# Performance work log

Measured on AMD Instinct MI355X. Metric: run time of the kernel, lower is better.

## Reference

```python
import jax, jax.numpy as jnp
import numpy as np

D_MODEL = 1024
N_HEADS = 16
HEAD_DIM = D_MODEL // N_HEADS  # 64
SCALE = HEAD_DIM ** -0.5       # nn.Parameter, frozen since lsa=False


def setup_inputs() -> dict:
    key = jax.random.key(0)
    kq, kk, kv = jax.random.split(key, 3)
    bs, h, s, d = 4, N_HEADS, 2048, HEAD_DIM
    q = jax.random.normal(kq, (bs, h, s, d), dtype=jnp.float32)
    k = jax.random.normal(kk, (bs, h, d, s), dtype=jnp.float32)  # pre-transposed like torch input
    v = jax.random.normal(kv, (bs, h, s, d), dtype=jnp.float32)
    return {"q": q, "k": k, "v": v}


def reference(q, k, v):
    # attn_scores: [bs, n_heads, q_len, seq_len]
    scale = jnp.asarray(SCALE, dtype=q.dtype)
    attn_scores = jnp.einsum('bhqd,bhds->bhqs', q, k) * scale
    # prev=None, attn_mask=None, key_padding_mask=None; dropout p=0.0 -> identity
    attn_weights = jax.nn.softmax(attn_scores, axis=-1)
    output = jnp.einsum('bhqs,bhsd->bhqd', attn_weights, v)
    return output, attn_weights
```

## Files before the change

### kernel.cpp

```cpp
#include <hip/hip_runtime.h>


#define S_LEN 2048
#define DH 64
#define NHEADS 64

typedef short short8 __attribute__((ext_vector_type(8)));
typedef float f32x4 __attribute__((ext_vector_type(4)));
typedef float f32x16 __attribute__((ext_vector_type(16)));
typedef unsigned short u16;

__device__ __forceinline__ u16 f2bf(float f) {
  union { float f; unsigned u; } x;
  x.f = f;
  unsigned r = x.u + 0x7fffu + ((x.u >> 16) & 1u);
  return (u16)(r >> 16);
}

__device__ __forceinline__ unsigned pkbf(float a, float b) {
  return (unsigned)f2bf(a) | ((unsigned)f2bf(b) << 16);
}

__device__ __forceinline__ void plswap(unsigned& a, unsigned& b) {
  asm("v_permlane32_swap_b32 %0, %1" : "+v"(a), "+v"(b));
}

__global__ __launch_bounds__(256) void cvt_scale_k(const float* __restrict__ in,
                                                   u16* __restrict__ out,
                                                   float scale, int n4) {
  int i = blockIdx.x * 256 + threadIdx.x;
  if (i >= n4) return;
  float4 v = ((const float4*)in)[i];
  union { u16 s[4]; unsigned long long ll; } o;
  o.s[0] = f2bf(v.x * scale); o.s[1] = f2bf(v.y * scale);
  o.s[2] = f2bf(v.z * scale); o.s[3] = f2bf(v.w * scale);
  ((unsigned long long*)out)[i] = o.ll;
}

__global__ __launch_bounds__(256) void transpose_cvt_k(const float* __restrict__ in,
                                                       u16* __restrict__ out,
                                                       int R, int C) {
  __shared__ float tile[64][65];
  const int tilesC = C >> 6;
  const int tilesPerHead = (R >> 6) * tilesC;
  int hb = blockIdx.x;
  int head = hb / tilesPerHead;
  int t = hb - head * tilesPerHead;
  int tr = t / tilesC, tc = t - tr * tilesC;
  const float* ip = in + (size_t)head * R * C + (size_t)tr * 64 * C + (size_t)tc * 64;
  u16* op = out + (size_t)head * R * C + (size_t)tc * 64 * R + (size_t)tr * 64;
  int c = threadIdx.x & 63, r0 = threadIdx.x >> 6;
#pragma unroll
  for (int k = 0; k < 16; ++k) {
    int r = (k << 2) + r0;
    tile[r][c] = ip[(size_t)r * C + c];
  }
  __syncthreads();
#pragma unroll
  for (int k = 0; k < 16; ++k) {
    int orow = (k << 2) + r0;
    op[(size_t)orow * R + c] = f2bf(tile[c][orow]);
  }
}

__global__ __launch_bounds__(256, 4) void attn_k(const u16* __restrict__ Qb,
                                                 const u16* __restrict__ Kn,
                                                 const u16* __restrict__ Vt,
                                                 float* __restrict__ Og,
                                                 float* __restrict__ Pg) {
  __shared__ float tile[4][32 * 32];
  int bid = blockIdx.x;
  int work = ((bid & 7) << 7) | (bid >> 3);
  int head = work >> 4;
  int rblk = work & 15;
  int lane = threadIdx.x & 63;
  int wv = threadIdx.x >> 6;
  int q = lane & 31;
  int hi = lane >> 5;
  int q0 = (rblk << 7) + (wv << 5);
  float* tw = tile[wv];
  int rq = lane >> 3;
  int rc = lane & 7;

  const u16* qp = Qb + (size_t)(head * S_LEN + q0 + q) * DH + hi * 8;
  short8 qf0 = *(const short8*)(qp);
  short8 qf1 = *(const short8*)(qp + 16);
  short8 qf2 = *(const short8*)(qp + 32);
  short8 qf3 = *(const short8*)(qp + 48);

  const u16* kp = Kn + (size_t)head * S_LEN * DH + (size_t)q * DH + hi * 8;
  const u16* vp = Vt + (size_t)head * DH * S_LEN + (size_t)q * S_LEN + hi * 8;

  float ls0 = 0.f, ls1 = 0.f, ls2 = 0.f, ls3 = 0.f;
  for (int j0 = 0; j0 < S_LEN; j0 += 32) {
    const u16* kb = kp + (size_t)j0 * DH;
    short8 k0 = *(const short8*)(kb);
    short8 k1 = *(const short8*)(kb + 16);
    short8 k2 = *(const short8*)(kb + 32);
    short8 k3 = *(const short8*)(kb + 48);
    f32x16 s = {};
    s = __builtin_amdgcn_mfma_f32_32x32x16_bf16(k0, qf0, s, 0, 0, 0);
    s = __builtin_amdgcn_mfma_f32_32x32x16_bf16(k1, qf1, s, 0, 0, 0);
    s = __builtin_amdgcn_mfma_f32_32x32x16_bf16(k2, qf2, s, 0, 0, 0);
    s = __builtin_amdgcn_mfma_f32_32x32x16_bf16(k3, qf3, s, 0, 0, 0);
#pragma unroll
    for (int r = 0; r < 16; r += 4) {
      ls0 += __expf(s[r]);
      ls1 += __expf(s[r + 1]);
      ls2 += __expf(s[r + 2]);
      ls3 += __expf(s[r + 3]);
    }
  }
  float ls = (ls0 + ls1) + (ls2 + ls3);
  ls += __shfl_xor(ls, 32);
  float rl = 1.f / ls;

  f32x16 oa = {}, ob = {};
  float* pbW = Pg + (size_t)(head * S_LEN + q0) * S_LEN;

  for (int j0 = 0; j0 < S_LEN; j0 += 32) {
    const u16* kb = kp + (size_t)j0 * DH;
    short8 k0 = *(const short8*)(kb);
    short8 k1 = *(const short8*)(kb + 16);
    short8 k2 = *(const short8*)(kb + 32);
    short8 k3 = *(const short8*)(kb + 48);
    const u16* vj = vp + j0;
    short8 v0 = *(const short8*)(vj);
    short8 v1 = *(const short8*)(vj + 16);
    short8 v2 = *(const short8*)(vj + 32 * S_LEN);
    short8 v3 = *(const short8*)(vj + 32 * S_LEN + 16);

    f32x16 s = {};
    s = __builtin_amdgcn_mfma_f32_32x32x16_bf16(k0, qf0, s, 0, 0, 0);
    s = __builtin_amdgcn_mfma_f32_32x32x16_bf16(k1, qf1, s, 0, 0, 0);
    s = __builtin_amdgcn_mfma_f32_32x32x16_bf16(k2, qf2, s, 0, 0, 0);
    s = __builtin_amdgcn_mfma_f32_32x32x16_bf16(k3, qf3, s, 0, 0, 0);

    float p[16];
#pragma unroll
    for (int r = 0; r < 16; ++r) p[r] = __expf(s[r]) * rl;

#pragma unroll
    for (int g = 0; g < 4; ++g) {
      int phys = (2 * g + hi) ^ (q & 7);
      f32x4 w = {p[4 * g], p[4 * g + 1], p[4 * g + 2], p[4 * g + 3]};
      *(f32x4*)&tw[q * 32 + phys * 4] = w;
    }

    unsigned A0 = pkbf(p[0], p[1]),   A1 = pkbf(p[2], p[3]);
    unsigned B0 = pkbf(p[4], p[5]),   B1 = pkbf(p[6], p[7]);
    plswap(A0, B0);
    plswap(A1, B1);
    unsigned C0 = pkbf(p[8], p[9]),   C1 = pkbf(p[10], p[11]);
    unsigned D0 = pkbf(p[12], p[13]), D1 = pkbf(p[14], p[15]);
    plswap(C0, D0);
    plswap(C1, D1);
    union { unsigned w[4]; short8 v; } pa0u = {{A0, A1, B0, B1}};
    union { unsigned w[4]; short8 v; } pa1u = {{C0, C1, D0, D1}};

    oa = __builtin_amdgcn_mfma_f32_32x32x16_bf16(pa0u.v, v0, oa, 0, 0, 0);
    oa = __builtin_amdgcn_mfma_f32_32x32x16_bf16(pa1u.v, v1, oa, 0, 0, 0);
    ob = __builtin_amdgcn_mfma_f32_32x32x16_bf16(pa0u.v, v2, ob, 0, 0, 0);
    ob = __builtin_amdgcn_mfma_f32_32x32x16_bf16(pa1u.v, v3, ob, 0, 0, 0);

    float* ps = pbW + j0;
#pragma unroll
    for (int g = 0; g < 4; ++g) {
      int qi = 8 * g + rq;
      int phys = rc ^ (qi & 7);
      f32x4 v = *(const f32x4*)&tw[qi * 32 + phys * 4];
      __builtin_nontemporal_store(v, (f32x4*)(ps + (size_t)qi * S_LEN + rc * 4));
    }
  }

  float* ogb = Og + (size_t)(head * S_LEN + q0) * DH;
#pragma unroll
  for (int r = 0; r < 16; ++r) {
    int qi = (r & 3) + 8 * (r >> 2) + 4 * hi;
    tw[qi * 32 + q] = oa[r];
  }
#pragma unroll
  for (int g = 0; g < 4; ++g) {
    int qi = 8 * g + rq;
    f32x4 v = *(const f32x4*)&tw[qi * 32 + rc * 4];
    __builtin_nontemporal_store(v, (f32x4*)(ogb + (size_t)qi * DH + rc * 4));
  }
#pragma unroll
  for (int r = 0; r < 16; ++r) {
    int qi = (r & 3) + 8 * (r >> 2) + 4 * hi;
    tw[qi * 32 + q] = ob[r];
  }
#pragma unroll
  for (int g = 0; g < 4; ++g) {
    int qi = 8 * g + rq;
    f32x4 v = *(const f32x4*)&tw[qi * 32 + rc * 4];
    __builtin_nontemporal_store(v, (f32x4*)(ogb + (size_t)qi * DH + 32 + rc * 4));
  }
}

extern "C" void kernel_launch(void* const* d_in, const int* in_sizes, int n_in,
                              void* d_out, int out_size, void* d_ws, size_t ws_size,
                              hipStream_t stream) {
  const float* q = (const float*)d_in[0];
  const float* k = (const float*)d_in[1];
  const float* v = (const float*)d_in[2];
  float* Og = (float*)d_out;
  float* Pg = Og + (size_t)NHEADS * S_LEN * DH;

  const size_t elems = (size_t)NHEADS * S_LEN * DH;
  u16* Qb = (u16*)d_ws;
  u16* Kn = Qb + elems;
  u16* Vt = Kn + elems;

  int n4 = (int)(elems / 4);
  cvt_scale_k<<<n4 / 256, 256, 0, stream>>>(q, Qb, 0.125f, n4);
  transpose_cvt_k<<<NHEADS * (S_LEN / 64), 256, 0, stream>>>(k, Kn, DH, S_LEN);
  transpose_cvt_k<<<NHEADS * (S_LEN / 64), 256, 0, stream>>>(v, Vt, S_LEN, DH);
  attn_k<<<NHEADS * (S_LEN / 128), 256, 0, stream>>>(Qb, Kn, Vt, Og, Pg);
}
```

Before: 406.5 us.

## Add dedicated store wavefront streaming attention probabilities from double-buffered LDS

Adds a fifth wavefront per block that only copies the softmax probability tiles from shared memory to global memory. The four compute wavefronts write their tiles into a double-buffered LDS area between two block barriers per iteration. The goal is to take the large global probability writes off the compute wavefronts' instruction stream so they overlap with the MFMA work. In exchange, it adds two block-wide barriers per key tile, doubles LDS use and concentrates all store issue in a single wavefront, which can become the limiter.

```diff
diff --git a/kernel.cpp b/kernel.cpp
--- a/kernel.cpp
+++ b/kernel.cpp
@@ -63,24 +63,46 @@
   }
 }
 
-__global__ __launch_bounds__(256, 4) void attn_k(const u16* __restrict__ Qb,
+__global__ __launch_bounds__(320, 5) void attn_k(const u16* __restrict__ Qb,
                                                  const u16* __restrict__ Kn,
                                                  const u16* __restrict__ Vt,
                                                  float* __restrict__ Og,
                                                  float* __restrict__ Pg) {
-  __shared__ float tile[4][32 * 32];
+  __shared__ float buf[2][4][32 * 32];
   int bid = blockIdx.x;
   int work = ((bid & 7) << 7) | (bid >> 3);
   int head = work >> 4;
   int rblk = work & 15;
   int lane = threadIdx.x & 63;
   int wv = threadIdx.x >> 6;
+  int rq = lane >> 3;
+  int rc = lane & 7;
+
+  if (wv == 4) {
+    float* pgb = Pg + ((size_t)head * S_LEN + (size_t)rblk * 128) * S_LEN;
+    for (int t = 0; t < 64; ++t) {
+      __syncthreads();
+      __syncthreads();
+      int j0 = t << 5;
+      const float* tb = &buf[t & 1][0][0];
+#pragma unroll
+      for (int w = 0; w < 4; ++w) {
+#pragma unroll
+        for (int g = 0; g < 4; ++g) {
+          int qi = 8 * g + rq;
+          int phys = rc ^ (qi & 7);
+          f32x4 v = *(const f32x4*)&tb[(w * 1024) + qi * 32 + phys * 4];
+          __builtin_nontemporal_store(
+              v, (f32x4*)(pgb + (size_t)(w * 32 + qi) * S_LEN + j0 + rc * 4));
+        }
+      }
+    }
+    return;
+  }
+
   int q = lane & 31;
   int hi = lane >> 5;
   int q0 = (rblk << 7) + (wv << 5);
-  float* tw = tile[wv];
-  int rq = lane >> 3;
-  int rc = lane & 7;
 
   const u16* qp = Qb + (size_t)(head * S_LEN + q0 + q) * DH + hi * 8;
   short8 qf0 = *(const short8*)(qp);
@@ -116,9 +138,9 @@
   float rl = 1.f / ls;
 
   f32x16 oa = {}, ob = {};
-  float* pbW = Pg + (size_t)(head * S_LEN + q0) * S_LEN;
-
-  for (int j0 = 0; j0 < S_LEN; j0 += 32) {
+
+  for (int t = 0; t < 64; ++t) {
+    int j0 = t << 5;
     const u16* kb = kp + (size_t)j0 * DH;
     short8 k0 = *(const short8*)(kb);
     short8 k1 = *(const short8*)(kb + 16);
@@ -140,12 +162,17 @@
 #pragma unroll
     for (int r = 0; r < 16; ++r) p[r] = __expf(s[r]) * rl;
 
+    __syncthreads();
+
+    float* tw = &buf[t & 1][wv][0];
 #pragma unroll
     for (int g = 0; g < 4; ++g) {
       int phys = (2 * g + hi) ^ (q & 7);
       f32x4 w = {p[4 * g], p[4 * g + 1], p[4 * g + 2], p[4 * g + 3]};
       *(f32x4*)&tw[q * 32 + phys * 4] = w;
     }
+
+    __syncthreads();
 
     unsigned A0 = pkbf(p[0], p[1]),   A1 = pkbf(p[2], p[3]);
     unsigned B0 = pkbf(p[4], p[5]),   B1 = pkbf(p[6], p[7]);
@@ -162,38 +189,30 @@
     oa = __builtin_amdgcn_mfma_f32_32x32x16_bf16(pa1u.v, v1, oa, 0, 0, 0);
     ob = __builtin_amdgcn_mfma_f32_32x32x16_bf16(pa0u.v, v2, ob, 0, 0, 0);
     ob = __builtin_amdgcn_mfma_f32_32x32x16_bf16(pa1u.v, v3, ob, 0, 0, 0);
-
-    float* ps = pbW + j0;
-#pragma unroll
-    for (int g = 0; g < 4; ++g) {
-      int qi = 8 * g + rq;
-      int phys = rc ^ (qi & 7);
-      f32x4 v = *(const f32x4*)&tw[qi * 32 + phys * 4];
-      __builtin_nontemporal_store(v, (f32x4*)(ps + (size_t)qi * S_LEN + rc * 4));
-    }
-  }
-
+  }
+
+  float* te = &buf[0][wv][0];
   float* ogb = Og + (size_t)(head * S_LEN + q0) * DH;
 #pragma unroll
   for (int r = 0; r < 16; ++r) {
     int qi = (r & 3) + 8 * (r >> 2) + 4 * hi;
-    tw[qi * 32 + q] = oa[r];
+    te[qi * 32 + q] = oa[r];
   }
 #pragma unroll
   for (int g = 0; g < 4; ++g) {
     int qi = 8 * g + rq;
-    f32x4 v = *(const f32x4*)&tw[qi * 32 + rc * 4];
+    f32x4 v = *(const f32x4*)&te[qi * 32 + rc * 4];
     __builtin_nontemporal_store(v, (f32x4*)(ogb + (size_t)qi * DH + rc * 4));
   }
 #pragma unroll
   for (int r = 0; r < 16; ++r) {
     int qi = (r & 3) + 8 * (r >> 2) + 4 * hi;
-    tw[qi * 32 + q] = ob[r];
+    te[qi * 32 + q] = ob[r];
   }
 #pragma unroll
   for (int g = 0; g < 4; ++g) {
     int qi = 8 * g + rq;
-    f32x4 v = *(const f32x4*)&tw[qi * 32 + rc * 4];
+    f32x4 v = *(const f32x4*)&te[qi * 32 + rc * 4];
     __builtin_nontemporal_store(v, (f32x4*)(ogb + (size_t)qi * DH + 32 + rc * 4));
   }
 }
@@ -216,5 +235,5 @@
   cvt_scale_k<<<n4 / 256, 256, 0, stream>>>(q, Qb, 0.125f, n4);
   transpose_cvt_k<<<NHEADS * (S_LEN / 64), 256, 0, stream>>>(k, Kn, DH, S_LEN);
   transpose_cvt_k<<<NHEADS * (S_LEN / 64), 256, 0, stream>>>(v, Vt, S_LEN, DH);
-  attn_k<<<NHEADS * (S_LEN / 128), 256, 0, stream>>>(Qb, Kn, Vt, Og, Pg);
-}
+  attn_k<<<NHEADS * (S_LEN / 128), 320, 0, stream>>>(Qb, Kn, Vt, Og, Pg);
+}
```

After: 466.8 us. +14.8%, slower.

## Process two query tiles per block, fusing second tile's row-sum pass into first's

Applied to the files above, without the earlier changes.

Each block now handles two 128-row query groups. The softmax-denominator pass for the second group is computed inside the first group's output loop, reusing the same K fragments, and the second group then runs its own output pass. This removes one separate QK^T sweep per pair of tiles and halves the grid, at the cost of higher register pressure (launch bounds lowered to 2 blocks) and fewer blocks for latency hiding.

```diff
diff --git a/kernel.cpp b/kernel.cpp
--- a/kernel.cpp
+++ b/kernel.cpp
@@ -63,35 +63,41 @@
   }
 }
 
-__global__ __launch_bounds__(256, 4) void attn_k(const u16* __restrict__ Qb,
+__global__ __launch_bounds__(256, 2) void attn_k(const u16* __restrict__ Qb,
                                                  const u16* __restrict__ Kn,
                                                  const u16* __restrict__ Vt,
                                                  float* __restrict__ Og,
                                                  float* __restrict__ Pg) {
   __shared__ float tile[4][32 * 32];
   int bid = blockIdx.x;
-  int work = ((bid & 7) << 7) | (bid >> 3);
-  int head = work >> 4;
-  int rblk = work & 15;
+  int work = ((bid & 7) << 6) | (bid >> 3);
+  int head = work >> 3;
+  int rblk = work & 7;
   int lane = threadIdx.x & 63;
   int wv = threadIdx.x >> 6;
   int q = lane & 31;
   int hi = lane >> 5;
-  int q0 = (rblk << 7) + (wv << 5);
+  int q0A = (rblk << 8) + (wv << 5);
+  int q0B = q0A + 128;
   float* tw = tile[wv];
   int rq = lane >> 3;
   int rc = lane & 7;
 
-  const u16* qp = Qb + (size_t)(head * S_LEN + q0 + q) * DH + hi * 8;
-  short8 qf0 = *(const short8*)(qp);
-  short8 qf1 = *(const short8*)(qp + 16);
-  short8 qf2 = *(const short8*)(qp + 32);
-  short8 qf3 = *(const short8*)(qp + 48);
+  const u16* qpA = Qb + (size_t)(head * S_LEN + q0A + q) * DH + hi * 8;
+  short8 qa0 = *(const short8*)(qpA);
+  short8 qa1 = *(const short8*)(qpA + 16);
+  short8 qa2 = *(const short8*)(qpA + 32);
+  short8 qa3 = *(const short8*)(qpA + 48);
+  const u16* qpB = Qb + (size_t)(head * S_LEN + q0B + q) * DH + hi * 8;
+  short8 qb0 = *(const short8*)(qpB);
+  short8 qb1 = *(const short8*)(qpB + 16);
+  short8 qb2 = *(const short8*)(qpB + 32);
+  short8 qb3 = *(const short8*)(qpB + 48);
 
   const u16* kp = Kn + (size_t)head * S_LEN * DH + (size_t)q * DH + hi * 8;
   const u16* vp = Vt + (size_t)head * DH * S_LEN + (size_t)q * S_LEN + hi * 8;
 
-  float ls0 = 0.f, ls1 = 0.f, ls2 = 0.f, ls3 = 0.f;
+  float la0 = 0.f, la1 = 0.f, la2 = 0.f, la3 = 0.f;
   for (int j0 = 0; j0 < S_LEN; j0 += 32) {
     const u16* kb = kp + (size_t)j0 * DH;
     short8 k0 = *(const short8*)(kb);
@@ -99,24 +105,25 @@
     short8 k2 = *(const short8*)(kb + 32);
     short8 k3 = *(const short8*)(kb + 48);
     f32x16 s = {};
-    s = __builtin_amdgcn_mfma_f32_32x32x16_bf16(k0, qf0, s, 0, 0, 0);
-    s = __builtin_amdgcn_mfma_f32_32x32x16_bf16(k1, qf1, s, 0, 0, 0);
-    s = __builtin_amdgcn_mfma_f32_32x32x16_bf16(k2, qf2, s, 0, 0, 0);
-    s = __builtin_amdgcn_mfma_f32_32x32x16_bf16(k3, qf3, s, 0, 0, 0);
+    s = __builtin_amdgcn_mfma_f32_32x32x16_bf16(k0, qa0, s, 0, 0, 0);
+    s = __builtin_amdgcn_mfma_f32_32x32x16_bf16(k1, qa1, s, 0, 0, 0);
+    s = __builtin_amdgcn_mfma_f32_32x32x16_bf16(k2, qa2, s, 0, 0, 0);
+    s = __builtin_amdgcn_mfma_f32_32x32x16_bf16(k3, qa3, s, 0, 0, 0);
 #pragma unroll
     for (int r = 0; r < 16; r += 4) {
-      ls0 += __expf(s[r]);
-      ls1 += __expf(s[r + 1]);
-      ls2 += __expf(s[r + 2]);
-      ls3 += __expf(s[r + 3]);
-    }
-  }
-  float ls = (ls0 + ls1) + (ls2 + ls3);
-  ls += __shfl_xor(ls, 32);
-  float rl = 1.f / ls;
+      la0 += __expf(s[r]);
+      la1 += __expf(s[r + 1]);
+      la2 += __expf(s[r + 2]);
+      la3 += __expf(s[r + 3]);
+    }
+  }
+  float lsA = (la0 + la1) + (la2 + la3);
+  lsA += __shfl_xor(lsA, 32);
+  float rlA = 1.f / lsA;
 
   f32x16 oa = {}, ob = {};
-  float* pbW = Pg + (size_t)(head * S_LEN + q0) * S_LEN;
+  float lb0 = 0.f, lb1 = 0.f, lb2 = 0.f, lb3 = 0.f;
+  float* pbA = Pg + (size_t)(head * S_LEN + q0A) * S_LEN;
 
   for (int j0 = 0; j0 < S_LEN; j0 += 32) {
     const u16* kb = kp + (size_t)j0 * DH;
@@ -131,14 +138,14 @@
     short8 v3 = *(const short8*)(vj + 32 * S_LEN + 16);
 
     f32x16 s = {};
-    s = __builtin_amdgcn_mfma_f32_32x32x16_bf16(k0, qf0, s, 0, 0, 0);
-    s = __builtin_amdgcn_mfma_f32_32x32x16_bf16(k1, qf1, s, 0, 0, 0);
-    s = __builtin_amdgcn_mfma_f32_32x32x16_bf16(k2, qf2, s, 0, 0, 0);
-    s = __builtin_amdgcn_mfma_f32_32x32x16_bf16(k3, qf3, s, 0, 0, 0);
+    s = __builtin_amdgcn_mfma_f32_32x32x16_bf16(k0, qa0, s, 0, 0, 0);
+    s = __builtin_amdgcn_mfma_f32_32x32x16_bf16(k1, qa1, s, 0, 0, 0);
+    s = __builtin_amdgcn_mfma_f32_32x32x16_bf16(k2, qa2, s, 0, 0, 0);
+    s = __builtin_amdgcn_mfma_f32_32x32x16_bf16(k3, qa3, s, 0, 0, 0);
 
     float p[16];
 #pragma unroll
-    for (int r = 0; r < 16; ++r) p[r] = __expf(s[r]) * rl;
+    for (int r = 0; r < 16; ++r) p[r] = __expf(s[r]) * rlA;
 
 #pragma unroll
     for (int g = 0; g < 4; ++g) {
@@ -163,7 +170,7 @@
     ob = __builtin_amdgcn_mfma_f32_32x32x16_bf16(pa0u.v, v2, ob, 0, 0, 0);
     ob = __builtin_amdgcn_mfma_f32_32x32x16_bf16(pa1u.v, v3, ob, 0, 0, 0);
 
-    float* ps = pbW + j0;
+    float* ps = pbA + j0;
 #pragma unroll
     for (int g = 0; g < 4; ++g) {
       int qi = 8 * g + rq;
@@ -171,9 +178,22 @@
       f32x4 v = *(const f32x4*)&tw[qi * 32 + phys * 4];
       __builtin_nontemporal_store(v, (f32x4*)(ps + (size_t)qi * S_LEN + rc * 4));
     }
-  }
-
-  float* ogb = Og + (size_t)(head * S_LEN + q0) * DH;
+
+    f32x16 sb = {};
+    sb = __builtin_amdgcn_mfma_f32_32x32x16_bf16(k0, qb0, sb, 0, 0, 0);
+    sb = __builtin_amdgcn_mfma_f32_32x32x16_bf16(k1, qb1, sb, 0, 0, 0);
+    sb = __builtin_amdgcn_mfma_f32_32x32x16_bf16(k2, qb2, sb, 0, 0, 0);
+    sb = __builtin_amdgcn_mfma_f32_32x32x16_bf16(k3, qb3, sb, 0, 0, 0);
+#pragma unroll
+    for (int r = 0; r < 16; r += 4) {
+      lb0 += __expf(sb[r]);
+      lb1 += __expf(sb[r + 1]);
+      lb2 += __expf(sb[r + 2]);
+      lb3 += __expf(sb[r + 3]);
+    }
+  }
+
+  float* ogA = Og + (size_t)(head * S_LEN + q0A) * DH;
 #pragma unroll
   for (int r = 0; r < 16; ++r) {
     int qi = (r & 3) + 8 * (r >> 2) + 4 * hi;
@@ -183,7 +203,7 @@
   for (int g = 0; g < 4; ++g) {
     int qi = 8 * g + rq;
     f32x4 v = *(const f32x4*)&tw[qi * 32 + rc * 4];
-    __builtin_nontemporal_store(v, (f32x4*)(ogb + (size_t)qi * DH + rc * 4));
+    __builtin_nontemporal_store(v, (f32x4*)(ogA + (size_t)qi * DH + rc * 4));
   }
 #pragma unroll
   for (int r = 0; r < 16; ++r) {
@@ -194,7 +214,94 @@
   for (int g = 0; g < 4; ++g) {
     int qi = 8 * g + rq;
     f32x4 v = *(const f32x4*)&tw[qi * 32 + rc * 4];
-    __builtin_nontemporal_store(v, (f32x4*)(ogb + (size_t)qi * DH + 32 + rc * 4));
+    __builtin_nontemporal_store(v, (f32x4*)(ogA + (size_t)qi * DH + 32 + rc * 4));
+  }
+
+  float lsB = (lb0 + lb1) + (lb2 + lb3);
+  lsB += __shfl_xor(lsB, 32);
+  float rlB = 1.f / lsB;
+
+  oa = (f32x16){};
+  ob = (f32x16){};
+  float* pbB = Pg + (size_t)(head * S_LEN + q0B) * S_LEN;
+
+  for (int j0 = 0; j0 < S_LEN; j0 += 32) {
+    const u16* kb = kp + (size_t)j0 * DH;
+    short8 k0 = *(const short8*)(kb);
+    short8 k1 = *(const short8*)(kb + 16);
+    short8 k2 = *(const short8*)(kb + 32);
+    short8 k3 = *(const short8*)(kb + 48);
+    const u16* vj = vp + j0;
+    short8 v0 = *(const short8*)(vj);
+    short8 v1 = *(const short8*)(vj + 16);
+    short8 v2 = *(const short8*)(vj + 32 * S_LEN);
+    short8 v3 = *(const short8*)(vj + 32 * S_LEN + 16);
+
+    f32x16 s = {};
+    s = __builtin_amdgcn_mfma_f32_32x32x16_bf16(k0, qb0, s, 0, 0, 0);
+    s = __builtin_amdgcn_mfma_f32_32x32x16_bf16(k1, qb1, s, 0, 0, 0);
+    s = __builtin_amdgcn_mfma_f32_32x32x16_bf16(k2, qb2, s, 0, 0, 0);
+    s = __builtin_amdgcn_mfma_f32_32x32x16_bf16(k3, qb3, s, 0, 0, 0);
+
+    float p[16];
+#pragma unroll
+    for (int r = 0; r < 16; ++r) p[r] = __expf(s[r]) * rlB;
+
+#pragma unroll
+    for (int g = 0; g < 4; ++g) {
+      int phys = (2 * g + hi) ^ (q & 7);
+      f32x4 w = {p[4 * g], p[4 * g + 1], p[4 * g + 2], p[4 * g + 3]};
+      *(f32x4*)&tw[q * 32 + phys * 4] = w;
+    }
+
+    unsigned A0 = pkbf(p[0], p[1]),   A1 = pkbf(p[2], p[3]);
+    unsigned B0 = pkbf(p[4], p[5]),   B1 = pkbf(p[6], p[7]);
+    plswap(A0, B0);
+    plswap(A1, B1);
+    unsigned C0 = pkbf(p[8], p[9]),   C1 = pkbf(p[10], p[11]);
+    unsigned D0 = pkbf(p[12], p[13]), D1 = pkbf(p[14], p[15]);
+    plswap(C0, D0);
+    plswap(C1, D1);
+    union { unsigned w[4]; short8 v; } pa0u = {{A0, A1, B0, B1}};
+    union { unsigned w[4]; short8 v; } pa1u = {{C0, C1, D0, D1}};
+
+    oa = __builtin_amdgcn_mfma_f32_32x32x16_bf16(pa0u.v, v0, oa, 0, 0, 0);
+    oa = __builtin_amdgcn_mfma_f32_32x32x16_bf16(pa1u.v, v1, oa, 0, 0, 0);
+    ob = __builtin_amdgcn_mfma_f32_32x32x16_bf16(pa0u.v, v2, ob, 0, 0, 0);
+    ob = __builtin_amdgcn_mfma_f32_32x32x16_bf16(pa1u.v, v3, ob, 0, 0, 0);
+
+    float* ps = pbB + j0;
+#pragma unroll
+    for (int g = 0; g < 4; ++g) {
+      int qi = 8 * g + rq;
+      int phys = rc ^ (qi & 7);
+      f32x4 v = *(const f32x4*)&tw[qi * 32 + phys * 4];
+      __builtin_nontemporal_store(v, (f32x4*)(ps + (size_t)qi * S_LEN + rc * 4));
+    }
+  }
+
+  float* ogB = Og + (size_t)(head * S_LEN + q0B) * DH;
+#pragma unroll
+  for (int r = 0; r < 16; ++r) {
+    int qi = (r & 3) + 8 * (r >> 2) + 4 * hi;
+    tw[qi * 32 + q] = oa[r];
+  }
+#pragma unroll
+  for (int g = 0; g < 4; ++g) {
+    int qi = 8 * g + rq;
+    f32x4 v = *(const f32x4*)&tw[qi * 32 + rc * 4];
+    __builtin_nontemporal_store(v, (f32x4*)(ogB + (size_t)qi * DH + rc * 4));
+  }
+#pragma unroll
+  for (int r = 0; r < 16; ++r) {
+    int qi = (r & 3) + 8 * (r >> 2) + 4 * hi;
+    tw[qi * 32 + q] = ob[r];
+  }
+#pragma unroll
+  for (int g = 0; g < 4; ++g) {
+    int qi = 8 * g + rq;
+    f32x4 v = *(const f32x4*)&tw[qi * 32 + rc * 4];
+    __builtin_nontemporal_store(v, (f32x4*)(ogB + (size_t)qi * DH + 32 + rc * 4));
   }
 }
 
@@ -216,5 +323,5 @@
   cvt_scale_k<<<n4 / 256, 256, 0, stream>>>(q, Qb, 0.125f, n4);
   transpose_cvt_k<<<NHEADS * (S_LEN / 64), 256, 0, stream>>>(k, Kn, DH, S_LEN);
   transpose_cvt_k<<<NHEADS * (S_LEN / 64), 256, 0, stream>>>(v, Vt, S_LEN, DH);
-  attn_k<<<NHEADS * (S_LEN / 128), 256, 0, stream>>>(Qb, Kn, Vt, Og, Pg);
-}
+  attn_k<<<NHEADS * (S_LEN / 256), 256, 0, stream>>>(Qb, Kn, Vt, Og, Pg);
+}
```

Measured after the change: 350.2 us. 1.16x faster.

## Software-pipeline softmax-denominator pass into previous tile's output pass across four query tiles

Applied to the files above, without the earlier changes.

Each 2-wave block now processes four 32-row query tiles per wave sequentially. The row-sum pass for the next tile is fused into the probability/PV pass of the current tile, so the K fragments loaded once serve both QK products. This removes most of the separate K re-read and the standalone first pass. The cost is lower occupancy (128 threads, launch bounds 1, half the blocks) and more registers from holding four Q tiles.

```diff
diff --git a/kernel.cpp b/kernel.cpp
--- a/kernel.cpp
+++ b/kernel.cpp
@@ -23,6 +23,31 @@
 
 __device__ __forceinline__ void plswap(unsigned& a, unsigned& b) {
   asm("v_permlane32_swap_b32 %0, %1" : "+v"(a), "+v"(b));
+}
+
+__device__ __forceinline__ f32x16 qk4(short8 k0, short8 k1, short8 k2, short8 k3,
+                                      short8 w0, short8 w1, short8 w2, short8 w3) {
+  f32x16 s = {};
+  s = __builtin_amdgcn_mfma_f32_32x32x16_bf16(k0, w0, s, 0, 0, 0);
+  s = __builtin_amdgcn_mfma_f32_32x32x16_bf16(k1, w1, s, 0, 0, 0);
+  s = __builtin_amdgcn_mfma_f32_32x32x16_bf16(k2, w2, s, 0, 0, 0);
+  s = __builtin_amdgcn_mfma_f32_32x32x16_bf16(k3, w3, s, 0, 0, 0);
+  return s;
+}
+
+__device__ __forceinline__ void packPA(const float* p, short8& f0, short8& f1) {
+  unsigned A0 = pkbf(p[0], p[1]),   A1 = pkbf(p[2], p[3]);
+  unsigned B0 = pkbf(p[4], p[5]),   B1 = pkbf(p[6], p[7]);
+  plswap(A0, B0);
+  plswap(A1, B1);
+  unsigned C0 = pkbf(p[8], p[9]),   C1 = pkbf(p[10], p[11]);
+  unsigned D0 = pkbf(p[12], p[13]), D1 = pkbf(p[14], p[15]);
+  plswap(C0, D0);
+  plswap(C1, D1);
+  union { unsigned w[4]; short8 v; } u0 = {{A0, A1, B0, B1}};
+  union { unsigned w[4]; short8 v; } u1 = {{C0, C1, D0, D1}};
+  f0 = u0.v;
+  f1 = u1.v;
 }
 
 __global__ __launch_bounds__(256) void cvt_scale_k(const float* __restrict__ in,
@@ -63,61 +88,37 @@
   }
 }
 
-__global__ __launch_bounds__(256, 4) void attn_k(const u16* __restrict__ Qb,
-                                                 const u16* __restrict__ Kn,
-                                                 const u16* __restrict__ Vt,
-                                                 float* __restrict__ Og,
-                                                 float* __restrict__ Pg) {
-  __shared__ float tile[4][32 * 32];
-  int bid = blockIdx.x;
-  int work = ((bid & 7) << 7) | (bid >> 3);
-  int head = work >> 4;
-  int rblk = work & 15;
-  int lane = threadIdx.x & 63;
-  int wv = threadIdx.x >> 6;
-  int q = lane & 31;
-  int hi = lane >> 5;
-  int q0 = (rblk << 7) + (wv << 5);
-  float* tw = tile[wv];
-  int rq = lane >> 3;
-  int rc = lane & 7;
-
-  const u16* qp = Qb + (size_t)(head * S_LEN + q0 + q) * DH + hi * 8;
-  short8 qf0 = *(const short8*)(qp);
-  short8 qf1 = *(const short8*)(qp + 16);
-  short8 qf2 = *(const short8*)(qp + 32);
-  short8 qf3 = *(const short8*)(qp + 48);
-
-  const u16* kp = Kn + (size_t)head * S_LEN * DH + (size_t)q * DH + hi * 8;
-  const u16* vp = Vt + (size_t)head * DH * S_LEN + (size_t)q * S_LEN + hi * 8;
-
-  float ls0 = 0.f, ls1 = 0.f, ls2 = 0.f, ls3 = 0.f;
+
+__device__ __forceinline__ float pass1_full(const u16* kp, short8 q0f, short8 q1f,
+                                            short8 q2f, short8 q3f) {
+  float l0 = 0.f, l1 = 0.f, l2 = 0.f, l3 = 0.f;
   for (int j0 = 0; j0 < S_LEN; j0 += 32) {
     const u16* kb = kp + (size_t)j0 * DH;
     short8 k0 = *(const short8*)(kb);
     short8 k1 = *(const short8*)(kb + 16);
     short8 k2 = *(const short8*)(kb + 32);
     short8 k3 = *(const short8*)(kb + 48);
-    f32x16 s = {};
-    s = __builtin_amdgcn_mfma_f32_32x32x16_bf16(k0, qf0, s, 0, 0, 0);
-    s = __builtin_amdgcn_mfma_f32_32x32x16_bf16(k1, qf1, s, 0, 0, 0);
-    s = __builtin_amdgcn_mfma_f32_32x32x16_bf16(k2, qf2, s, 0, 0, 0);
-    s = __builtin_amdgcn_mfma_f32_32x32x16_bf16(k3, qf3, s, 0, 0, 0);
+    f32x16 s = qk4(k0, k1, k2, k3, q0f, q1f, q2f, q3f);
 #pragma unroll
     for (int r = 0; r < 16; r += 4) {
-      ls0 += __expf(s[r]);
-      ls1 += __expf(s[r + 1]);
-      ls2 += __expf(s[r + 2]);
-      ls3 += __expf(s[r + 3]);
-    }
-  }
-  float ls = (ls0 + ls1) + (ls2 + ls3);
+      l0 += __expf(s[r]);
+      l1 += __expf(s[r + 1]);
+      l2 += __expf(s[r + 2]);
+      l3 += __expf(s[r + 3]);
+    }
+  }
+  float ls = (l0 + l1) + (l2 + l3);
   ls += __shfl_xor(ls, 32);
-  float rl = 1.f / ls;
-
-  f32x16 oa = {}, ob = {};
-  float* pbW = Pg + (size_t)(head * S_LEN + q0) * S_LEN;
-
+  return 1.f / ls;
+}
+
+__device__ __forceinline__ void fused_phase(
+    const u16* kp, const u16* vp, float* tw, float* pbase,
+    short8 qa0, short8 qa1, short8 qa2, short8 qa3, float rl,
+    short8 qb0, short8 qb1, short8 qb2, short8 qb3,
+    f32x16& oa, f32x16& ob, float& lnext,
+    int q, int hi, int rq, int rc) {
+  float lb0 = 0.f, lb1 = 0.f, lb2 = 0.f, lb3 = 0.f;
   for (int j0 = 0; j0 < S_LEN; j0 += 32) {
     const u16* kb = kp + (size_t)j0 * DH;
     short8 k0 = *(const short8*)(kb);
@@ -130,12 +131,7 @@
     short8 v2 = *(const short8*)(vj + 32 * S_LEN);
     short8 v3 = *(const short8*)(vj + 32 * S_LEN + 16);
 
-    f32x16 s = {};
-    s = __builtin_amdgcn_mfma_f32_32x32x16_bf16(k0, qf0, s, 0, 0, 0);
-    s = __builtin_amdgcn_mfma_f32_32x32x16_bf16(k1, qf1, s, 0, 0, 0);
-    s = __builtin_amdgcn_mfma_f32_32x32x16_bf16(k2, qf2, s, 0, 0, 0);
-    s = __builtin_amdgcn_mfma_f32_32x32x16_bf16(k3, qf3, s, 0, 0, 0);
-
+    f32x16 s = qk4(k0, k1, k2, k3, qa0, qa1, qa2, qa3);
     float p[16];
 #pragma unroll
     for (int r = 0; r < 16; ++r) p[r] = __expf(s[r]) * rl;
@@ -147,23 +143,23 @@
       *(f32x4*)&tw[q * 32 + phys * 4] = w;
     }
 
-    unsigned A0 = pkbf(p[0], p[1]),   A1 = pkbf(p[2], p[3]);
-    unsigned B0 = pkbf(p[4], p[5]),   B1 = pkbf(p[6], p[7]);
-    plswap(A0, B0);
-    plswap(A1, B1);
-    unsigned C0 = pkbf(p[8], p[9]),   C1 = pkbf(p[10], p[11]);
-    unsigned D0 = pkbf(p[12], p[13]), D1 = pkbf(p[14], p[15]);
-    plswap(C0, D0);
-    plswap(C1, D1);
-    union { unsigned w[4]; short8 v; } pa0u = {{A0, A1, B0, B1}};
-    union { unsigned w[4]; short8 v; } pa1u = {{C0, C1, D0, D1}};
-
-    oa = __builtin_amdgcn_mfma_f32_32x32x16_bf16(pa0u.v, v0, oa, 0, 0, 0);
-    oa = __builtin_amdgcn_mfma_f32_32x32x16_bf16(pa1u.v, v1, oa, 0, 0, 0);
-    ob = __builtin_amdgcn_mfma_f32_32x32x16_bf16(pa0u.v, v2, ob, 0, 0, 0);
-    ob = __builtin_amdgcn_mfma_f32_32x32x16_bf16(pa1u.v, v3, ob, 0, 0, 0);
-
-    float* ps = pbW + j0;
+    short8 pa0, pa1;
+    packPA(p, pa0, pa1);
+    oa = __builtin_amdgcn_mfma_f32_32x32x16_bf16(pa0, v0, oa, 0, 0, 0);
+    oa = __builtin_amdgcn_mfma_f32_32x32x16_bf16(pa1, v1, oa, 0, 0, 0);
+    ob = __builtin_amdgcn_mfma_f32_32x32x16_bf16(pa0, v2, ob, 0, 0, 0);
+    ob = __builtin_amdgcn_mfma_f32_32x32x16_bf16(pa1, v3, ob, 0, 0, 0);
+
+    f32x16 sb = qk4(k0, k1, k2, k3, qb0, qb1, qb2, qb3);
+#pragma unroll
+    for (int r = 0; r < 16; r += 4) {
+      lb0 += __expf(sb[r]);
+      lb1 += __expf(sb[r + 1]);
+      lb2 += __expf(sb[r + 2]);
+      lb3 += __expf(sb[r + 3]);
+    }
+
+    float* ps = pbase + j0;
 #pragma unroll
     for (int g = 0; g < 4; ++g) {
       int qi = 8 * g + rq;
@@ -172,8 +168,60 @@
       __builtin_nontemporal_store(v, (f32x4*)(ps + (size_t)qi * S_LEN + rc * 4));
     }
   }
-
-  float* ogb = Og + (size_t)(head * S_LEN + q0) * DH;
+  float ls = (lb0 + lb1) + (lb2 + lb3);
+  ls += __shfl_xor(ls, 32);
+  lnext = 1.f / ls;
+}
+
+__device__ __forceinline__ void pass2_only(
+    const u16* kp, const u16* vp, float* tw, float* pbase,
+    short8 qa0, short8 qa1, short8 qa2, short8 qa3, float rl,
+    f32x16& oa, f32x16& ob, int q, int hi, int rq, int rc) {
+  for (int j0 = 0; j0 < S_LEN; j0 += 32) {
+    const u16* kb = kp + (size_t)j0 * DH;
+    short8 k0 = *(const short8*)(kb);
+    short8 k1 = *(const short8*)(kb + 16);
+    short8 k2 = *(const short8*)(kb + 32);
+    short8 k3 = *(const short8*)(kb + 48);
+    const u16* vj = vp + j0;
+    short8 v0 = *(const short8*)(vj);
+    short8 v1 = *(const short8*)(vj + 16);
+    short8 v2 = *(const short8*)(vj + 32 * S_LEN);
+    short8 v3 = *(const short8*)(vj + 32 * S_LEN + 16);
+
+    f32x16 s = qk4(k0, k1, k2, k3, qa0, qa1, qa2, qa3);
+    float p[16];
+#pragma unroll
+    for (int r = 0; r < 16; ++r) p[r] = __expf(s[r]) * rl;
+
+#pragma unroll
+    for (int g = 0; g < 4; ++g) {
+      int phys = (2 * g + hi) ^ (q & 7);
+      f32x4 w = {p[4 * g], p[4 * g + 1], p[4 * g + 2], p[4 * g + 3]};
+      *(f32x4*)&tw[q * 32 + phys * 4] = w;
+    }
+
+    short8 pa0, pa1;
+    packPA(p, pa0, pa1);
+    oa = __builtin_amdgcn_mfma_f32_32x32x16_bf16(pa0, v0, oa, 0, 0, 0);
+    oa = __builtin_amdgcn_mfma_f32_32x32x16_bf16(pa1, v1, oa, 0, 0, 0);
+    ob = __builtin_amdgcn_mfma_f32_32x32x16_bf16(pa0, v2, ob, 0, 0, 0);
+    ob = __builtin_amdgcn_mfma_f32_32x32x16_bf16(pa1, v3, ob, 0, 0, 0);
+
+    float* ps = pbase + j0;
+#pragma unroll
+    for (int g = 0; g < 4; ++g) {
+      int qi = 8 * g + rq;
+      int phys = rc ^ (qi & 7);
+      f32x4 v = *(const f32x4*)&tw[qi * 32 + phys * 4];
+      __builtin_nontemporal_store(v, (f32x4*)(ps + (size_t)qi * S_LEN + rc * 4));
+    }
+  }
+}
+
+__device__ __forceinline__ void o_epilogue(float* tw, const f32x16& oa,
+                                           const f32x16& ob, float* og,
+                                           int q, int hi, int rq, int rc) {
 #pragma unroll
   for (int r = 0; r < 16; ++r) {
     int qi = (r & 3) + 8 * (r >> 2) + 4 * hi;
@@ -183,7 +231,7 @@
   for (int g = 0; g < 4; ++g) {
     int qi = 8 * g + rq;
     f32x4 v = *(const f32x4*)&tw[qi * 32 + rc * 4];
-    __builtin_nontemporal_store(v, (f32x4*)(ogb + (size_t)qi * DH + rc * 4));
+    __builtin_nontemporal_store(v, (f32x4*)(og + (size_t)qi * DH + rc * 4));
   }
 #pragma unroll
   for (int r = 0; r < 16; ++r) {
@@ -194,8 +242,74 @@
   for (int g = 0; g < 4; ++g) {
     int qi = 8 * g + rq;
     f32x4 v = *(const f32x4*)&tw[qi * 32 + rc * 4];
-    __builtin_nontemporal_store(v, (f32x4*)(ogb + (size_t)qi * DH + 32 + rc * 4));
-  }
+    __builtin_nontemporal_store(v, (f32x4*)(og + (size_t)qi * DH + 32 + rc * 4));
+  }
+}
+
+__global__ __launch_bounds__(128, 1) void attn_k(const u16* __restrict__ Qb,
+                                                 const u16* __restrict__ Kn,
+                                                 const u16* __restrict__ Vt,
+                                                 float* __restrict__ Og,
+                                                 float* __restrict__ Pg) {
+  __shared__ float tile[2][32 * 32];
+  int bid = blockIdx.x;
+  int work = ((bid & 7) << 6) | (bid >> 3);
+  int head = work >> 3;
+  int rblk = work & 7;
+  int lane = threadIdx.x & 63;
+  int wv = threadIdx.x >> 6;
+  int q = lane & 31;
+  int hi = lane >> 5;
+  float* tw = tile[wv];
+  int rq = lane >> 3;
+  int rc = lane & 7;
+
+  int base = (rblk << 8) + (wv << 5);
+  int q0A = base, q0B = base + 64, q0C = base + 128, q0D = base + 192;
+
+  const u16* qh = Qb + (size_t)head * S_LEN * DH;
+  const u16* qpA = qh + (size_t)(q0A + q) * DH + hi * 8;
+  short8 qa0 = *(const short8*)(qpA),      qa1 = *(const short8*)(qpA + 16);
+  short8 qa2 = *(const short8*)(qpA + 32), qa3 = *(const short8*)(qpA + 48);
+  const u16* qpB = qh + (size_t)(q0B + q) * DH + hi * 8;
+  short8 qb0 = *(const short8*)(qpB),      qb1 = *(const short8*)(qpB + 16);
+  short8 qb2 = *(const short8*)(qpB + 32), qb3 = *(const short8*)(qpB + 48);
+  const u16* qpC = qh + (size_t)(q0C + q) * DH + hi * 8;
+  short8 qc0 = *(const short8*)(qpC),      qc1 = *(const short8*)(qpC + 16);
+  short8 qc2 = *(const short8*)(qpC + 32), qc3 = *(const short8*)(qpC + 48);
+  const u16* qpD = qh + (size_t)(q0D + q) * DH + hi * 8;
+  short8 qd0 = *(const short8*)(qpD),      qd1 = *(const short8*)(qpD + 16);
+  short8 qd2 = *(const short8*)(qpD + 32), qd3 = *(const short8*)(qpD + 48);
+
+  const u16* kp = Kn + (size_t)head * S_LEN * DH + (size_t)q * DH + hi * 8;
+  const u16* vp = Vt + (size_t)head * DH * S_LEN + (size_t)q * S_LEN + hi * 8;
+  float* ph = Pg + (size_t)head * S_LEN * S_LEN;
+  float* oh = Og + (size_t)head * S_LEN * DH;
+
+  float rlA = pass1_full(kp, qa0, qa1, qa2, qa3);
+
+  f32x16 oa = {}, ob = {};
+  float rlB;
+  fused_phase(kp, vp, tw, ph + (size_t)q0A * S_LEN, qa0, qa1, qa2, qa3, rlA,
+              qb0, qb1, qb2, qb3, oa, ob, rlB, q, hi, rq, rc);
+  o_epilogue(tw, oa, ob, oh + (size_t)q0A * DH, q, hi, rq, rc);
+
+  oa = (f32x16){}; ob = (f32x16){};
+  float rlC;
+  fused_phase(kp, vp, tw, ph + (size_t)q0B * S_LEN, qb0, qb1, qb2, qb3, rlB,
+              qc0, qc1, qc2, qc3, oa, ob, rlC, q, hi, rq, rc);
+  o_epilogue(tw, oa, ob, oh + (size_t)q0B * DH, q, hi, rq, rc);
+
+  oa = (f32x16){}; ob = (f32x16){};
+  float rlD;
+  fused_phase(kp, vp, tw, ph + (size_t)q0C * S_LEN, qc0, qc1, qc2, qc3, rlC,
+              qd0, qd1, qd2, qd3, oa, ob, rlD, q, hi, rq, rc);
+  o_epilogue(tw, oa, ob, oh + (size_t)q0C * DH, q, hi, rq, rc);
+
+  oa = (f32x16){}; ob = (f32x16){};
+  pass2_only(kp, vp, tw, ph + (size_t)q0D * S_LEN, qd0, qd1, qd2, qd3, rlD,
+             oa, ob, q, hi, rq, rc);
+  o_epilogue(tw, oa, ob, oh + (size_t)q0D * DH, q, hi, rq, rc);
 }
 
 extern "C" void kernel_launch(void* const* d_in, const int* in_sizes, int n_in,
@@ -216,5 +330,5 @@
   cvt_scale_k<<<n4 / 256, 256, 0, stream>>>(q, Qb, 0.125f, n4);
   transpose_cvt_k<<<NHEADS * (S_LEN / 64), 256, 0, stream>>>(k, Kn, DH, S_LEN);
   transpose_cvt_k<<<NHEADS * (S_LEN / 64), 256, 0, stream>>>(v, Vt, S_LEN, DH);
-  attn_k<<<NHEADS * (S_LEN / 128), 256, 0, stream>>>(Qb, Kn, Vt, Og, Pg);
-}
+  attn_k<<<NHEADS * (S_LEN / 256), 128, 0, stream>>>(Qb, Kn, Vt, Og, Pg);
+}
```

After: 362.5 us. 1.12x faster.
